# Performance work log

Hardware: AMD Instinct MI355X
Metric: run time of the kernel (lower is better)

The kernel has to match this reference:

```python
import jax, jax.numpy as jnp
import numpy as np

B, N = 4, 512
H, NH, L = 64, 4, 3
HD = H // NH          # 16
NODE_F, EDGE_F = 18, 7
H4 = H // 4           # 16
FF = 4 * H            # 256


def _ln(x, g, b, eps=1e-5):
    m = jnp.mean(x, axis=-1, keepdims=True)
    v = jnp.mean((x - m) ** 2, axis=-1, keepdims=True)
    return (x - m) * jax.lax.rsqrt(v + eps) * g + b


def _leaky(x):
    return jnp.where(x >= 0, x, 0.2 * x)


def _spd(edge_mask):
    # Vectorized Floyd-Warshall, mirrors GraphTransformer._compute_spd_matrix
    n = edge_mask.shape[1]
    spd = jnp.where(edge_mask, 1.0, float(n)).astype(jnp.float32)
    i = jnp.arange(n)
    spd = spd.at[:, i, i].set(0.0)
    def body(k, s):
        col = jax.lax.dynamic_slice_in_dim(s, k, 1, axis=2)  # [B,N,1]
        row = jax.lax.dynamic_slice_in_dim(s, k, 1, axis=1)  # [B,1,N]
        return jnp.minimum(s, col + row)
    return jax.lax.fori_loop(0, n, body, spd)


def setup_inputs() -> dict:
    key = jax.random.key(0)
    ks = iter(jax.random.split(key, 64))
    def nrm(shape, s):
        return jax.random.normal(next(ks), shape, jnp.float32) * s
    inp = {}
    inp["node_features"] = jax.random.normal(next(ks), (B, N, NODE_F), jnp.float32)
    inp["edge_features"] = jax.random.normal(next(ks), (B, N, N, EDGE_F), jnp.float32)
    nm = jax.random.uniform(next(ks), (B, N)) < 0.9
    inp["node_mask"] = nm.at[:, 0].set(True)
    inp["edge_mask"] = jax.random.uniform(next(ks), (B, N, N)) < 0.05
    s_h = 1.0 / np.sqrt(H)
    inp["node_proj_w"] = nrm((NODE_F, H), 0.2)
    inp["node_proj_b"] = jnp.zeros((H,), jnp.float32)
    inp["edge_proj_w"] = nrm((EDGE_F, H), 0.2)
    inp["edge_proj_b"] = jnp.zeros((H,), jnp.float32)
    inp["wq"] = nrm((L, H, H), s_h)
    inp["wk"] = nrm((L, H, H), s_h)
    inp["wv"] = nrm((L, H, H), s_h)
    inp["eb1_w"] = nrm((L, H, H4), s_h)
    inp["eb1_b"] = jnp.zeros((L, H4), jnp.float32)
    inp["eb_ln_g"] = jnp.ones((L, H4), jnp.float32)
    inp["eb_ln_b"] = jnp.zeros((L, H4), jnp.float32)
    inp["eb2_w"] = nrm((L, H4, NH), 0.2)
    inp["eb2_b"] = jnp.zeros((L, NH), jnp.float32)
    inp["spd1_w"] = nrm((L, 1, H4), 0.5)
    inp["spd1_b"] = jnp.zeros((L, H4), jnp.float32)
    inp["spd2_w"] = nrm((L, H4, NH), 0.2)
    inp["spd2_b"] = jnp.zeros((L, NH), jnp.float32)
    inp["wo_w"] = nrm((L, H, H), s_h)
    inp["wo_b"] = jnp.zeros((L, H), jnp.float32)
    inp["ln1_g"] = jnp.ones((L, H), jnp.float32)
    inp["ln1_b"] = jnp.zeros((L, H), jnp.float32)
    inp["ln2_g"] = jnp.ones((L, H), jnp.float32)
    inp["ln2_b"] = jnp.zeros((L, H), jnp.float32)
    inp["ffn1_w"] = nrm((L, H, FF), s_h)
    inp["ffn1_b"] = jnp.zeros((L, FF), jnp.float32)
    inp["ffn2_w"] = nrm((L, FF, H), 1.0 / np.sqrt(FF))
    inp["ffn2_b"] = jnp.zeros((L, H), jnp.float32)
    inp["score1_w"] = nrm((2 * H, H), 1.0 / np.sqrt(2 * H))
    inp["score1_b"] = jnp.zeros((H,), jnp.float32)
    inp["score_ln_g"] = jnp.ones((H,), jnp.float32)
    inp["score_ln_b"] = jnp.zeros((H,), jnp.float32)
    inp["score2_w"] = nrm((H, 1), 0.1)
    inp["score2_b"] = jnp.zeros((1,), jnp.float32)
    return inp


def reference(node_features, edge_features, node_mask, edge_mask,
              node_proj_w, node_proj_b, edge_proj_w, edge_proj_b,
              wq, wk, wv,
              eb1_w, eb1_b, eb_ln_g, eb_ln_b, eb2_w, eb2_b,
              spd1_w, spd1_b, spd2_w, spd2_b,
              wo_w, wo_b, ln1_g, ln1_b, ln2_g, ln2_b,
              ffn1_w, ffn1_b, ffn2_w, ffn2_b,
              score1_w, score1_b, score_ln_g, score_ln_b, score2_w, score2_b):
    NEG = -1000000000.0
    h = node_features @ node_proj_w + node_proj_b            # [B,N,H]
    e = edge_features @ edge_proj_w + edge_proj_b            # [B,N,N,H]
    spd = _spd(edge_mask)
    spd_n = (jnp.clip(spd, 0.0, 10.0) / 10.0)[..., None]      # [B,N,N,1]
    scale = 1.0 / np.sqrt(HD)
    for l in range(L):
        Q = (h @ wq[l]).reshape(B, N, NH, HD)
        K = (h @ wk[l]).reshape(B, N, NH, HD)
        V = (h @ wv[l]).reshape(B, N, NH, HD)
        scores = jnp.einsum('bihd,bjhd->bhij', Q, K) * scale  # [B,NH,N,N]
        x = _leaky(_ln(e @ eb1_w[l] + eb1_b[l], eb_ln_g[l], eb_ln_b[l]))
        edge_bias = jnp.transpose(x @ eb2_w[l] + eb2_b[l], (0, 3, 1, 2))
        sb = _leaky(spd_n @ spd1_w[l] + spd1_b[l]) @ spd2_w[l] + spd2_b[l]
        spd_bias = jnp.transpose(sb, (0, 3, 1, 2))
        bias = jnp.where(edge_mask[:, None, :, :], edge_bias, spd_bias)
        scores = jnp.where(node_mask[:, None, None, :], scores + bias, NEG)
        attn = jax.nn.softmax(scores, axis=-1)
        out = jnp.einsum('bhij,bjhd->bihd', attn, V).reshape(B, N, H)
        out = out @ wo_w[l] + wo_b[l]
        h = _ln(h + out, ln1_g[l], ln1_b[l])
        ff = jax.nn.gelu(h @ ffn1_w[l] + ffn1_b[l], approximate=False) @ ffn2_w[l] + ffn2_b[l]
        h = _ln(h + ff, ln2_g[l], ln2_b[l])
    h_ego = jnp.broadcast_to(h[:, :1, :], (B, N - 1, H))
    hc = jnp.concatenate([h_ego, h[:, 1:, :]], axis=-1)       # [B,N-1,2H]
    x = _leaky(_ln(hc @ score1_w + score1_b, score_ln_g, score_ln_b))
    logits = (x @ score2_w + score2_b)[..., 0]                # [B,N-1]
    cand_mask = node_mask[:, 1:]
    no_cand = ~jnp.any(cand_mask, axis=-1)
    cand_mask = cand_mask.at[:, 0].set(cand_mask[:, 0] | no_cand)
    logits = jnp.where(cand_mask, logits, NEG)
    probs = jax.nn.softmax(logits, axis=-1)
    return probs, h
```

## Files before the change

### kernel.cpp

```cpp
#include <hip/hip_runtime.h>
#include <math.h>

#define BB 4
#define NN 512
#define HH 64
#define NHH 4
#define HDD 16
#define LL 3
#define NNSQ 262144
#define FFF 256

__device__ __forceinline__ float wsum(float x) {
#pragma unroll
    for (int o = 1; o < 64; o <<= 1) x += __shfl_xor(x, o);
    return x;
}
__device__ __forceinline__ float wmaxr(float x) {
#pragma unroll
    for (int o = 1; o < 64; o <<= 1) x = fmaxf(x, __shfl_xor(x, o));
    return x;
}

__global__ void k_adj(const int* __restrict__ em, unsigned long long* __restrict__ adj,
                      unsigned int* __restrict__ blockCnt) {
    __shared__ unsigned int wc[4];
    int wv = threadIdx.x >> 6, lane = threadIdx.x & 63;
    int wid = blockIdx.x * 4 + wv;
    int chunk = wid & 7;
    int row = wid >> 3;
    int j = chunk * 64 + lane;
    int v = em[(size_t)row * NN + j];
    unsigned long long bal = __ballot(v != 0);
    if (lane == 0) { adj[row * 8 + chunk] = bal; wc[wv] = (unsigned int)__popcll(bal); }
    __syncthreads();
    if (threadIdx.x == 0) blockCnt[blockIdx.x] = wc[0] + wc[1] + wc[2] + wc[3];
}

__global__ void k_bfs(const unsigned long long* __restrict__ adj, unsigned char* __restrict__ spd) {
    __shared__ unsigned long long vis[8], fro[8], nxt[8];
    __shared__ unsigned long long dist8[64];
    unsigned char* dist = (unsigned char*)dist8;
    int t = threadIdx.x;
    int row = blockIdx.x;
    int b = row >> 9; int src = row & 511;
    dist8[t] = 0x0A0A0A0A0A0A0A0AULL;
    if (t < 8) { vis[t] = 0ULL; fro[t] = 0ULL; }
    __syncthreads();
    if (t == 0) {
        dist[src] = 0;
        vis[src >> 6] = 1ULL << (src & 63);
        fro[src >> 6] = 1ULL << (src & 63);
    }
    __syncthreads();
    const unsigned long long* arow = adj + (size_t)b * NN * 8;
    for (int d = 1; d <= 9; d++) {
        if (t < 8) nxt[t] = 0ULL;
        __syncthreads();
        int c = t >> 3, w = t & 7;
        unsigned long long f = fro[c];
        unsigned long long acc = 0ULL;
        while (f) {
            int k = (c << 6) + __builtin_ctzll(f);
            f &= f - 1;
            acc |= arow[k * 8 + w];
        }
        if (acc) atomicOr(&nxt[w], acc);
        __syncthreads();
        if (t < 8) {
            unsigned long long nw = nxt[t] & ~vis[t];
            vis[t] |= nw;
            fro[t] = nw;
            while (nw) {
                int j = (t << 6) + __builtin_ctzll(nw);
                nw &= nw - 1;
                dist[j] = (unsigned char)d;
            }
        }
        __syncthreads();
    }
    ((unsigned long long*)(spd + (size_t)row * NN))[t] = dist8[t];
}

__global__ __launch_bounds__(1024) void k_scan(const unsigned int* __restrict__ blockCnt,
                                               unsigned int* __restrict__ blockOff,
                                               unsigned int* __restrict__ counter) {
    __shared__ unsigned int part[1024];
    int t = threadIdx.x;
    unsigned int v0 = blockCnt[t * 4], v1 = blockCnt[t * 4 + 1],
                 v2 = blockCnt[t * 4 + 2], v3 = blockCnt[t * 4 + 3];
    unsigned int s = v0 + v1 + v2 + v3;
    part[t] = s;
    __syncthreads();
    for (int o = 1; o < 1024; o <<= 1) {
        unsigned int add = (t >= o) ? part[t - o] : 0u;
        __syncthreads();
        part[t] += add;
        __syncthreads();
    }
    unsigned int excl = part[t] - s;
    blockOff[t * 4]     = excl;
    blockOff[t * 4 + 1] = excl + v0;
    blockOff[t * 4 + 2] = excl + v0 + v1;
    blockOff[t * 4 + 3] = excl + v0 + v1 + v2;
    if (t == 1023) { counter[0] = part[t]; blockOff[4096] = part[t]; }
}

__global__ void k_scatter(const int* __restrict__ em, const unsigned int* __restrict__ blockOff,
                          unsigned int* __restrict__ elist) {
    __shared__ unsigned int wc[4];
    int t = threadIdx.x; int lane = t & 63; int wv = t >> 6;
    int idx = blockIdx.x * 256 + t;
    bool m = em[idx] != 0;
    unsigned long long bal = __ballot(m);
    if (lane == 0) wc[wv] = (unsigned int)__popcll(bal);
    __syncthreads();
    unsigned int base = blockOff[blockIdx.x];
    for (int w = 0; w < wv; w++) base += wc[w];
    if (m) {
        int pre = __popcll(bal & ((1ULL << lane) - 1ULL));
        elist[base + pre] = (unsigned int)idx;
    }
}

__global__ __launch_bounds__(256) void k_edge_bias(
    const float* __restrict__ ef, const unsigned int* __restrict__ counter,
    const unsigned int* __restrict__ elist,
    const float* __restrict__ epw, const float* __restrict__ epb,
    const float* __restrict__ eb1w, const float* __restrict__ eb1b,
    const float* __restrict__ lng, const float* __restrict__ lnb,
    const float* __restrict__ eb2w, const float* __restrict__ eb2b,
    float* __restrict__ vals) {
    unsigned int count = *counter;
    unsigned int idx = blockIdx.x * 256 + threadIdx.x;
    if (idx >= count) return;
    int l = blockIdx.y;
    unsigned int pos = elist[idx];
    const float* e7 = ef + (size_t)pos * 7;
    float f0 = e7[0], f1 = e7[1], f2 = e7[2], f3 = e7[3], f4 = e7[4], f5 = e7[5], f6 = e7[6];
    float tt[16];
#pragma unroll
    for (int c = 0; c < 16; c++) tt[c] = eb1b[l * 16 + c];
    const float* W1 = eb1w + l * 1024;
    for (int k = 0; k < 64; k++) {
        float ek = epb[k] + f0 * epw[k] + f1 * epw[64 + k] + f2 * epw[128 + k] + f3 * epw[192 + k]
                 + f4 * epw[256 + k] + f5 * epw[320 + k] + f6 * epw[384 + k];
#pragma unroll
        for (int c = 0; c < 16; c++) tt[c] += ek * W1[k * 16 + c];
    }
    float m = 0.f;
#pragma unroll
    for (int c = 0; c < 16; c++) m += tt[c];
    m *= 0.0625f;
    float var = 0.f;
#pragma unroll
    for (int c = 0; c < 16; c++) { float d = tt[c] - m; var += d * d; }
    var *= 0.0625f;
    float inv = rsqrtf(var + 1e-5f);
#pragma unroll
    for (int c = 0; c < 16; c++) {
        float x = (tt[c] - m) * inv * lng[l * 16 + c] + lnb[l * 16 + c];
        tt[c] = x >= 0.f ? x : 0.2f * x;
    }
#pragma unroll
    for (int hh = 0; hh < 4; hh++) {
        float a = eb2b[l * 4 + hh];
#pragma unroll
        for (int c = 0; c < 16; c++) a += tt[c] * eb2w[(l * 16 + c) * 4 + hh];
        vals[(unsigned int)((l * 4 + hh) << 16) + idx] = a;
    }
}

__global__ void k_node_proj(const float* __restrict__ nf, const float* __restrict__ w,
                            const float* __restrict__ bb, float* __restrict__ h) {
    int wid = blockIdx.x * 4 + (threadIdx.x >> 6);
    int f = threadIdx.x & 63;
    const float* r = nf + (size_t)wid * 18;
    float acc = bb[f];
#pragma unroll
    for (int c = 0; c < 18; c++) acc += r[c] * w[c * 64 + f];
    h[(size_t)wid * 64 + f] = acc;
}

__global__ __launch_bounds__(256) void k_qkvT(
    const float* __restrict__ h,
    const float* __restrict__ WQ, const float* __restrict__ WK, const float* __restrict__ WV,
    float* __restrict__ Q, float* __restrict__ KT, float* __restrict__ VT) {
    __shared__ float h_lds[16][64];
    int t = threadIdx.x;
    size_t base = (size_t)blockIdx.x * 16 * 64;
    for (int u = t; u < 1024; u += 256) ((float*)h_lds)[u] = h[base + u];
    __syncthreads();
    int wv = t >> 6, lane = t & 63;
    float aq[4] = {0,0,0,0}, ak[4] = {0,0,0,0}, av[4] = {0,0,0,0};
    for (int k = 0; k < 64; k++) {
        float wqv = WQ[k * 64 + lane], wkv = WK[k * 64 + lane], wvv = WV[k * 64 + lane];
#pragma unroll
        for (int r = 0; r < 4; r++) {
            float hv = h_lds[wv * 4 + r][k];
            aq[r] += hv * wqv; ak[r] += hv * wkv; av[r] += hv * wvv;
        }
    }
#pragma unroll
    for (int r = 0; r < 4; r++) {
        Q[base + (size_t)(wv * 4 + r) * 64 + lane] = aq[r];
    }
    int b = blockIdx.x >> 5;
    int j0 = (blockIdx.x & 31) * 16 + wv * 4;
    float4 kk; kk.x = ak[0]; kk.y = ak[1]; kk.z = ak[2]; kk.w = ak[3];
    float4 vv; vv.x = av[0]; vv.y = av[1]; vv.z = av[2]; vv.w = av[3];
    *(float4*)(KT + ((size_t)(b * 64 + lane)) * 512 + j0) = kk;
    *(float4*)(VT + ((size_t)(b * 64 + lane)) * 512 + j0) = vv;
}

__global__ __launch_bounds__(256) void k_attn3(
    const float* __restrict__ Q, const float* __restrict__ KT, const float* __restrict__ VT,
    const unsigned char* __restrict__ spd, const unsigned int* __restrict__ elist,
    const unsigned int* __restrict__ rowOff, const float* __restrict__ vals,
    const float* __restrict__ s1w, const float* __restrict__ s1b,
    const float* __restrict__ s2w, const float* __restrict__ s2b,
    const int* __restrict__ nmask, int l, float* __restrict__ attO) {
    __shared__ float kt[8192];
    __shared__ float bv[8192];
    __shared__ float tab[11];
    int bh = blockIdx.x;
    int b  = bh >> 2, hh = bh & 3;
    int i0 = blockIdx.y * 16;
    int t = threadIdx.x, wv = t >> 6, lane = t & 63;
    int rbase = i0 + wv * 4;
    float qv = Q[((size_t)(b * 512 + rbase + (lane >> 4))) * 64 + hh * 16 + (lane & 15)];
    float q[4][16];
#pragma unroll
    for (int r = 0; r < 4; r++)
#pragma unroll
        for (int d = 0; d < 16; d++)
            q[r][d] = __shfl(qv, r * 16 + d);
    const float4* ktg = (const float4*)(KT + (size_t)bh * 8192);
    float4* kts = (float4*)kt;
#pragma unroll
    for (int u = 0; u < 8; u++) kts[t + u * 256] = ktg[t + u * 256];
    if (t < 11) {
        float x = (float)t * 0.1f;
        float acc = s2b[l * 4 + hh];
#pragma unroll
        for (int c = 0; c < 16; c++) {
            float v = x * s1w[l * 16 + c] + s1b[l * 16 + c];
            v = v >= 0.f ? v : 0.2f * v;
            acc += v * s2w[(l * 16 + c) * 4 + hh];
        }
        tab[t] = acc;
    }
    __syncthreads();
    const unsigned char* sp = spd + ((size_t)(b * 512 + i0)) * 512;
#pragma unroll
    for (int u = 0; u < 8; u++) {
        int e4 = u * 1024 + t * 4;
        unsigned int w4 = *(const unsigned int*)(sp + e4);
        bv[e4 + 0] = tab[w4 & 255u];
        bv[e4 + 1] = tab[(w4 >> 8) & 255u];
        bv[e4 + 2] = tab[(w4 >> 16) & 255u];
        bv[e4 + 3] = tab[w4 >> 24];
    }
    __syncthreads();
    unsigned int vplane = (unsigned int)((l * 4 + hh) << 16);
#pragma unroll
    for (int rr = 0; rr < 4; rr++) {
        int g = b * 512 + rbase + rr;
        unsigned int e0 = rowOff[2 * g], e1 = rowOff[2 * g + 2];
        for (unsigned int e = e0 + lane; e < e1; e += 64) {
            int j = (int)(elist[e] & 511u);
            bv[(wv * 4 + rr) * 512 + j] = vals[vplane + e];
        }
    }
    __syncthreads();
    const int* nmb = nmask + b * 512;
    float sc[8][4];
    float mx[4] = {-3e38f, -3e38f, -3e38f, -3e38f};
#pragma unroll
    for (int c = 0; c < 8; c++) {
        int j = c * 64 + lane;
        float ktv[16];
#pragma unroll
        for (int d = 0; d < 16; d++) ktv[d] = kt[d * 512 + j];
        float madd = (nmb[j] != 0) ? 0.f : -1e9f;
#pragma unroll
        for (int r = 0; r < 4; r++) {
            float s = 0.f;
#pragma unroll
            for (int d = 0; d < 16; d++) s += q[r][d] * ktv[d];
            s = s * 0.25f + bv[(wv * 4 + r) * 512 + j] + madd;
            sc[c][r] = s;
            mx[r] = fmaxf(mx[r], s);
        }
    }
#pragma unroll
    for (int r = 0; r < 4; r++) mx[r] = wmaxr(mx[r]);
    float sm[4] = {0.f, 0.f, 0.f, 0.f};
#pragma unroll
    for (int c = 0; c < 8; c++)
#pragma unroll
        for (int r = 0; r < 4; r++) { sc[c][r] = __expf(sc[c][r] - mx[r]); sm[r] += sc[c][r]; }
#pragma unroll
    for (int r = 0; r < 4; r++) sm[r] = 1.0f / wsum(sm[r]);
#pragma unroll
    for (int c = 0; c < 8; c++)
#pragma unroll
        for (int r = 0; r < 4; r++) sc[c][r] *= sm[r];
    __syncthreads();
    const float4* vtg = (const float4*)(VT + (size_t)bh * 8192);
    float4* vts = (float4*)bv;
#pragma unroll
    for (int u = 0; u < 8; u++) vts[t + u * 256] = vtg[t + u * 256];
    __syncthreads();
    float acc[4][16];
#pragma unroll
    for (int r = 0; r < 4; r++)
#pragma unroll
        for (int d = 0; d < 16; d++) acc[r][d] = 0.f;
#pragma unroll
    for (int c = 0; c < 8; c++) {
        int j = c * 64 + lane;
#pragma unroll
        for (int d = 0; d < 16; d++) {
            float v = bv[d * 512 + j];
#pragma unroll
            for (int r = 0; r < 4; r++) acc[r][d] += sc[c][r] * v;
        }
    }
#pragma unroll
    for (int r = 0; r < 4; r++)
#pragma unroll
        for (int d = 0; d < 16; d++) {
            acc[r][d] += __shfl_xor(acc[r][d], 16);
            acc[r][d] += __shfl_xor(acc[r][d], 32);
        }
    __syncthreads();
    float* scr = kt + wv * 1040;
    if (lane < 16) {
#pragma unroll
        for (int r = 0; r < 4; r++)
#pragma unroll
            for (int d = 0; d < 16; d++) scr[lane * 65 + r * 16 + d] = acc[r][d];
    }
    float o = 0.f;
#pragma unroll
    for (int m = 0; m < 16; m++) o += scr[m * 65 + lane];
    attO[((size_t)(b * 512 + rbase + (lane >> 4))) * 64 + hh * 16 + (lane & 15)] = o;
}

__global__ __launch_bounds__(256) void k_oproj_ln1(
    const float* __restrict__ attO, const float* __restrict__ W, const float* __restrict__ Wb,
    const float* __restrict__ G, const float* __restrict__ Bt,
    float* __restrict__ h) {
    __shared__ float a_lds[4][64];
    int wv = threadIdx.x >> 6, lane = threadIdx.x & 63;
    int row = blockIdx.x * 4 + wv;
    a_lds[wv][lane] = attO[(size_t)row * 64 + lane];
    __syncthreads();
    float acc = Wb[lane];
#pragma unroll 8
    for (int k = 0; k < 64; k++) acc += a_lds[wv][k] * W[k * 64 + lane];
    float x = acc + h[(size_t)row * 64 + lane];
    float mn = wsum(x) * 0.015625f;
    float d = x - mn;
    float var = wsum(d * d) * 0.015625f;
    h[(size_t)row * 64 + lane] = d * rsqrtf(var + 1e-5f) * G[lane] + Bt[lane];
}

__global__ __launch_bounds__(256) void k_ffn(
    const float* __restrict__ W1, const float* __restrict__ B1,
    const float* __restrict__ W2, const float* __restrict__ B2,
    const float* __restrict__ G, const float* __restrict__ Bt,
    float* __restrict__ h) {
    __shared__ float h_lds[16][64];
    __shared__ float ff_lds[16][256];
    int t = threadIdx.x;
    size_t base = (size_t)blockIdx.x * 16 * 64;
    for (int u = t; u < 1024; u += 256) ((float*)h_lds)[u] = h[base + u];
    __syncthreads();
    int wv = t >> 6, lane = t & 63;
    float acc[4][4];
#pragma unroll
    for (int m = 0; m < 4; m++) {
        float bvv = B1[m * 64 + lane];
#pragma unroll
        for (int r = 0; r < 4; r++) acc[m][r] = bvv;
    }
    for (int k = 0; k < 64; k++) {
        float w0 = W1[k * 256 + lane], w1 = W1[k * 256 + 64 + lane],
              w2 = W1[k * 256 + 128 + lane], w3 = W1[k * 256 + 192 + lane];
#pragma unroll
        for (int r = 0; r < 4; r++) {
            float hv = h_lds[wv * 4 + r][k];
            acc[0][r] += hv * w0; acc[1][r] += hv * w1;
            acc[2][r] += hv * w2; acc[3][r] += hv * w3;
        }
    }
#pragma unroll
    for (int m = 0; m < 4; m++)
#pragma unroll
        for (int r = 0; r < 4; r++) {
            float u = acc[m][r];
            ff_lds[wv * 4 + r][m * 64 + lane] = 0.5f * u * (1.0f + erff(u * 0.70710678118654752f));
        }
    __syncthreads();
    float a2[4] = {0,0,0,0};
    for (int k = 0; k < 256; k++) {
        float w = W2[k * 64 + lane];
#pragma unroll
        for (int r = 0; r < 4; r++) a2[r] += ff_lds[wv * 4 + r][k] * w;
    }
    float b2v = B2[lane], gv = G[lane], btv = Bt[lane];
#pragma unroll
    for (int r = 0; r < 4; r++) {
        float x = a2[r] + b2v + h_lds[wv * 4 + r][lane];
        float mn = wsum(x) * 0.015625f;
        float d = x - mn;
        float var = wsum(d * d) * 0.015625f;
        h[base + (size_t)(wv * 4 + r) * 64 + lane] = d * rsqrtf(var + 1e-5f) * gv + btv;
    }
}

__global__ __launch_bounds__(256) void k_score(
    const float* __restrict__ h, const float* __restrict__ s1w, const float* __restrict__ s1b,
    const float* __restrict__ lng, const float* __restrict__ lnb,
    const float* __restrict__ s2w, const float* __restrict__ s2b,
    float* __restrict__ logits) {
    __shared__ float c_lds[4][128];
    int wv = threadIdx.x >> 6, lane = threadIdx.x & 63;
    int wid = blockIdx.x * 4 + wv;
    int b = wid / 511; int jj = wid % 511; int j = jj + 1;
    c_lds[wv][lane]      = h[((size_t)b * 512) * 64 + lane];
    c_lds[wv][64 + lane] = h[((size_t)(b * 512 + j)) * 64 + lane];
    __syncthreads();
    float acc = s1b[lane];
#pragma unroll 8
    for (int k = 0; k < 128; k++) acc += c_lds[wv][k] * s1w[k * 64 + lane];
    float mn = wsum(acc) * 0.015625f;
    float d = acc - mn;
    float var = wsum(d * d) * 0.015625f;
    float x = d * rsqrtf(var + 1e-5f) * lng[lane] + lnb[lane];
    x = x >= 0.f ? x : 0.2f * x;
    float p = wsum(x * s2w[lane]);
    if (lane == 0) logits[wid] = p + s2b[0];
}

__global__ __launch_bounds__(512) void k_probs(
    const float* __restrict__ logits, const int* __restrict__ nmask, float* __restrict__ out) {
    __shared__ float red[512];
    __shared__ int anyf;
    int b = blockIdx.x; int t = threadIdx.x;
    bool cand = false;
    if (t < 511) cand = nmask[b * 512 + 1 + t] != 0;
    if (t == 0) anyf = 0;
    __syncthreads();
    if (cand) atomicOr(&anyf, 1);
    __syncthreads();
    if (t == 0 && anyf == 0) cand = true;
    float val = -3e38f;
    if (t < 511) val = cand ? logits[b * 511 + t] : -1e9f;
    red[t] = val; __syncthreads();
    for (int s = 256; s > 0; s >>= 1) { if (t < s) red[t] = fmaxf(red[t], red[t + s]); __syncthreads(); }
    float m = red[0]; __syncthreads();
    float p = (t < 511) ? __expf(val - m) : 0.f;
    red[t] = p; __syncthreads();
    for (int s = 256; s > 0; s >>= 1) { if (t < s) red[t] += red[t + s]; __syncthreads(); }
    float inv = 1.0f / red[0];
    if (t < 511) out[b * 511 + t] = p * inv;
}

__global__ void k_copy_h(const float4* __restrict__ src, float4* __restrict__ dst) {
    int i = blockIdx.x * 256 + threadIdx.x;
    dst[i] = src[i];
}

extern "C" void kernel_launch(void* const* d_in, const int* in_sizes, int n_in,
                              void* d_out, int out_size, void* d_ws, size_t ws_size,
                              hipStream_t stream) {
    const float* nf    = (const float*)d_in[0];
    const float* ef    = (const float*)d_in[1];
    const int*   nm    = (const int*)d_in[2];
    const int*   em    = (const int*)d_in[3];
    const float* npw   = (const float*)d_in[4];
    const float* npb   = (const float*)d_in[5];
    const float* epw   = (const float*)d_in[6];
    const float* epb   = (const float*)d_in[7];
    const float* wq    = (const float*)d_in[8];
    const float* wk    = (const float*)d_in[9];
    const float* wv    = (const float*)d_in[10];
    const float* eb1w  = (const float*)d_in[11];
    const float* eb1b  = (const float*)d_in[12];
    const float* eblng = (const float*)d_in[13];
    const float* eblnb = (const float*)d_in[14];
    const float* eb2w  = (const float*)d_in[15];
    const float* eb2b  = (const float*)d_in[16];
    const float* s1wv  = (const float*)d_in[17];
    const float* s1bv  = (const float*)d_in[18];
    const float* s2wv  = (const float*)d_in[19];
    const float* s2bv  = (const float*)d_in[20];
    const float* wow   = (const float*)d_in[21];
    const float* wob   = (const float*)d_in[22];
    const float* ln1g  = (const float*)d_in[23];
    const float* ln1b  = (const float*)d_in[24];
    const float* ln2g  = (const float*)d_in[25];
    const float* ln2b  = (const float*)d_in[26];
    const float* f1w   = (const float*)d_in[27];
    const float* f1b   = (const float*)d_in[28];
    const float* f2w   = (const float*)d_in[29];
    const float* f2b   = (const float*)d_in[30];
    const float* sc1w  = (const float*)d_in[31];
    const float* sc1b  = (const float*)d_in[32];
    const float* sclng = (const float*)d_in[33];
    const float* sclnb = (const float*)d_in[34];
    const float* sc2w  = (const float*)d_in[35];
    const float* sc2b  = (const float*)d_in[36];

    char* W = (char*)d_ws;
    unsigned long long* adj     = (unsigned long long*)(W + 0);
    unsigned char*      spd     = (unsigned char*)(W + 131072);
    unsigned int*       counter = (unsigned int*)(W + 1179648);
    unsigned int*       elist   = (unsigned int*)(W + 1179904);
    float*              vals    = (float*)(W + 5374208);
    float*              hbuf    = (float*)(W + 8519936);
    float*              Qb      = (float*)(W + 9044224);
    float*              KTb     = (float*)(W + 9568512);
    float*              VTb     = (float*)(W + 10092800);
    float*              attO    = (float*)(W + 10617088);
    float*              logits  = (float*)(W + 11141376);
    unsigned int*       blockCnt= (unsigned int*)(W + 11149568);
    unsigned int*       blockOff= (unsigned int*)(W + 11165952);

    float* out = (float*)d_out;

    k_adj<<<4096, 256, 0, stream>>>(em, adj, blockCnt);
    k_bfs<<<2048, 64, 0, stream>>>(adj, spd);
    k_scan<<<1, 1024, 0, stream>>>(blockCnt, blockOff, counter);
    k_scatter<<<4096, 256, 0, stream>>>(em, blockOff, elist);
    k_edge_bias<<<dim3(256, 3), 256, 0, stream>>>(ef, counter, elist, epw, epb,
                                                  eb1w, eb1b, eblng, eblnb, eb2w, eb2b, vals);
    k_node_proj<<<512, 256, 0, stream>>>(nf, npw, npb, hbuf);

    for (int l = 0; l < LL; l++) {
        k_qkvT<<<128, 256, 0, stream>>>(hbuf, wq + l * 4096, wk + l * 4096, wv + l * 4096,
                                        Qb, KTb, VTb);
        k_attn3<<<dim3(16, 32), 256, 0, stream>>>(Qb, KTb, VTb, spd, elist, blockOff, vals,
                                                  s1wv, s1bv, s2wv, s2bv, nm, l, attO);
        k_oproj_ln1<<<512, 256, 0, stream>>>(attO, wow + l * 4096, wob + l * 64,
                                             ln1g + l * 64, ln1b + l * 64, hbuf);
        k_ffn<<<128, 256, 0, stream>>>(f1w + l * 16384, f1b + l * 256,
                                       f2w + l * 16384, f2b + l * 64,
                                       ln2g + l * 64, ln2b + l * 64, hbuf);
    }

    k_score<<<511, 256, 0, stream>>>(hbuf, sc1w, sc1b, sclng, sclnb, sc2w, sc2b, logits);
    k_copy_h<<<128, 256, 0, stream>>>((const float4*)hbuf, (float4*)(out + 2044));
    k_probs<<<4, 512, 0, stream>>>(logits, nm, out);
}
```

Measured before the change: 348.4 us.

## Fuse node projection, O-proj+LN1+FFN, output copy; widen BFS to 256 threads

The node projection is folded into the first-layer QKV kernel. The output projection with LayerNorm1 is merged into the FFN kernel, and the final copy of h is written directly from the last layer's FFN epilogue. Together these remove several kernel launches and global round-trips of the hidden state. The BFS kernel moves from 64 to 256 threads per block, scanning frontier bits per node instead of ctz loops over the frontier, and writes distances in parallel. The BFS change adds work proportional to all 512 nodes per level and more syncs, and the fused post kernel runs only 128 blocks.

New measurement: 366.6 us. 1.05x slower.

```diff
diff --git a/kernel.cpp b/kernel.cpp
--- a/kernel.cpp
+++ b/kernel.cpp
@@ -36,49 +36,46 @@
     if (threadIdx.x == 0) blockCnt[blockIdx.x] = wc[0] + wc[1] + wc[2] + wc[3];
 }
 
-__global__ void k_bfs(const unsigned long long* __restrict__ adj, unsigned char* __restrict__ spd) {
+__global__ __launch_bounds__(256) void k_bfs(const unsigned long long* __restrict__ adj,
+                                             unsigned char* __restrict__ spd) {
     __shared__ unsigned long long vis[8], fro[8], nxt[8];
     __shared__ unsigned long long dist8[64];
     unsigned char* dist = (unsigned char*)dist8;
     int t = threadIdx.x;
     int row = blockIdx.x;
     int b = row >> 9; int src = row & 511;
-    dist8[t] = 0x0A0A0A0A0A0A0A0AULL;
-    if (t < 8) { vis[t] = 0ULL; fro[t] = 0ULL; }
+    if (t < 64) dist8[t] = 0x0A0A0A0A0A0A0A0AULL;
+    if (t < 8) { vis[t] = 0ULL; fro[t] = 0ULL; nxt[t] = 0ULL; }
     __syncthreads();
     if (t == 0) {
         dist[src] = 0;
-        vis[src >> 6] = 1ULL << (src & 63);
-        fro[src >> 6] = 1ULL << (src & 63);
+        vis[src >> 6] |= 1ULL << (src & 63);
+        fro[src >> 6] |= 1ULL << (src & 63);
     }
     __syncthreads();
     const unsigned long long* arow = adj + (size_t)b * NN * 8;
+    int w = t & 7;
     for (int d = 1; d <= 9; d++) {
-        if (t < 8) nxt[t] = 0ULL;
-        __syncthreads();
-        int c = t >> 3, w = t & 7;
-        unsigned long long f = fro[c];
-        unsigned long long acc = 0ULL;
-        while (f) {
-            int k = (c << 6) + __builtin_ctzll(f);
-            f &= f - 1;
-            acc |= arow[k * 8 + w];
-        }
-        if (acc) atomicOr(&nxt[w], acc);
+        for (int k = t >> 3; k < 512; k += 32) {
+            if ((fro[k >> 6] >> (k & 63)) & 1ULL) {
+                unsigned long long m = arow[k * 8 + w];
+                if (m) atomicOr(&nxt[w], m);
+            }
+        }
         __syncthreads();
         if (t < 8) {
             unsigned long long nw = nxt[t] & ~vis[t];
             vis[t] |= nw;
             fro[t] = nw;
-            while (nw) {
-                int j = (t << 6) + __builtin_ctzll(nw);
-                nw &= nw - 1;
-                dist[j] = (unsigned char)d;
-            }
+            nxt[t] = 0ULL;
         }
         __syncthreads();
-    }
-    ((unsigned long long*)(spd + (size_t)row * NN))[t] = dist8[t];
+        for (int k = t; k < 512; k += 256) {
+            if ((fro[k >> 6] >> (k & 63)) & 1ULL) dist[k] = (unsigned char)d;
+        }
+        __syncthreads();
+    }
+    if (t < 64) ((unsigned long long*)(spd + (size_t)row * NN))[t] = dist8[t];
 }
 
 __global__ __launch_bounds__(1024) void k_scan(const unsigned int* __restrict__ blockCnt,
@@ -170,25 +167,30 @@
     }
 }
 
-__global__ void k_node_proj(const float* __restrict__ nf, const float* __restrict__ w,
-                            const float* __restrict__ bb, float* __restrict__ h) {
-    int wid = blockIdx.x * 4 + (threadIdx.x >> 6);
-    int f = threadIdx.x & 63;
-    const float* r = nf + (size_t)wid * 18;
-    float acc = bb[f];
-#pragma unroll
-    for (int c = 0; c < 18; c++) acc += r[c] * w[c * 64 + f];
-    h[(size_t)wid * 64 + f] = acc;
-}
-
 __global__ __launch_bounds__(256) void k_qkvT(
-    const float* __restrict__ h,
+    const float* __restrict__ h, const float* __restrict__ nf,
+    const float* __restrict__ npw, const float* __restrict__ npb,
     const float* __restrict__ WQ, const float* __restrict__ WK, const float* __restrict__ WV,
-    float* __restrict__ Q, float* __restrict__ KT, float* __restrict__ VT) {
+    float* __restrict__ Q, float* __restrict__ KT, float* __restrict__ VT,
+    float* __restrict__ hOut, int first) {
     __shared__ float h_lds[16][64];
+    __shared__ float nf_lds[16][18];
     int t = threadIdx.x;
     size_t base = (size_t)blockIdx.x * 16 * 64;
-    for (int u = t; u < 1024; u += 256) ((float*)h_lds)[u] = h[base + u];
+    if (first) {
+        for (int u = t; u < 288; u += 256) nf_lds[u / 18][u % 18] = nf[(size_t)blockIdx.x * 288 + u];
+        __syncthreads();
+        for (int u = t; u < 1024; u += 256) {
+            int row = u >> 6, col = u & 63;
+            float acc = npb[col];
+#pragma unroll
+            for (int c = 0; c < 18; c++) acc += nf_lds[row][c] * npw[c * 64 + col];
+            h_lds[row][col] = acc;
+            hOut[base + u] = acc;
+        }
+    } else {
+        for (int u = t; u < 1024; u += 256) ((float*)h_lds)[u] = h[base + u];
+    }
     __syncthreads();
     int wv = t >> 6, lane = t & 63;
     float aq[4] = {0,0,0,0}, ak[4] = {0,0,0,0}, av[4] = {0,0,0,0};
@@ -347,37 +349,38 @@
     attO[((size_t)(b * 512 + rbase + (lane >> 4))) * 64 + hh * 16 + (lane & 15)] = o;
 }
 
-__global__ __launch_bounds__(256) void k_oproj_ln1(
-    const float* __restrict__ attO, const float* __restrict__ W, const float* __restrict__ Wb,
-    const float* __restrict__ G, const float* __restrict__ Bt,
-    float* __restrict__ h) {
-    __shared__ float a_lds[4][64];
-    int wv = threadIdx.x >> 6, lane = threadIdx.x & 63;
-    int row = blockIdx.x * 4 + wv;
-    a_lds[wv][lane] = attO[(size_t)row * 64 + lane];
-    __syncthreads();
-    float acc = Wb[lane];
-#pragma unroll 8
-    for (int k = 0; k < 64; k++) acc += a_lds[wv][k] * W[k * 64 + lane];
-    float x = acc + h[(size_t)row * 64 + lane];
-    float mn = wsum(x) * 0.015625f;
-    float d = x - mn;
-    float var = wsum(d * d) * 0.015625f;
-    h[(size_t)row * 64 + lane] = d * rsqrtf(var + 1e-5f) * G[lane] + Bt[lane];
-}
-
-__global__ __launch_bounds__(256) void k_ffn(
+__global__ __launch_bounds__(256) void k_post(
+    const float* __restrict__ attO,
+    const float* __restrict__ Wo, const float* __restrict__ Wob,
+    const float* __restrict__ G1, const float* __restrict__ B1n,
     const float* __restrict__ W1, const float* __restrict__ B1,
     const float* __restrict__ W2, const float* __restrict__ B2,
-    const float* __restrict__ G, const float* __restrict__ Bt,
-    float* __restrict__ h) {
+    const float* __restrict__ G2, const float* __restrict__ Bt2,
+    float* __restrict__ h, float* __restrict__ outH) {
+    __shared__ float a_lds[16][64];
     __shared__ float h_lds[16][64];
     __shared__ float ff_lds[16][256];
     int t = threadIdx.x;
     size_t base = (size_t)blockIdx.x * 16 * 64;
-    for (int u = t; u < 1024; u += 256) ((float*)h_lds)[u] = h[base + u];
+    for (int u = t; u < 1024; u += 256) {
+        ((float*)a_lds)[u] = attO[base + u];
+        ((float*)h_lds)[u] = h[base + u];
+    }
     __syncthreads();
     int wv = t >> 6, lane = t & 63;
+#pragma unroll
+    for (int rr = 0; rr < 4; rr++) {
+        int row = wv * 4 + rr;
+        float acc = Wob[lane];
+#pragma unroll 8
+        for (int k = 0; k < 64; k++) acc += a_lds[row][k] * Wo[k * 64 + lane];
+        float x = acc + h_lds[row][lane];
+        float mn = wsum(x) * 0.015625f;
+        float d = x - mn;
+        float var = wsum(d * d) * 0.015625f;
+        h_lds[row][lane] = d * rsqrtf(var + 1e-5f) * G1[lane] + B1n[lane];
+    }
+    __syncthreads();
     float acc[4][4];
 #pragma unroll
     for (int m = 0; m < 4; m++) {
@@ -409,14 +412,17 @@
 #pragma unroll
         for (int r = 0; r < 4; r++) a2[r] += ff_lds[wv * 4 + r][k] * w;
     }
-    float b2v = B2[lane], gv = G[lane], btv = Bt[lane];
+    float b2v = B2[lane], gv = G2[lane], btv = Bt2[lane];
 #pragma unroll
     for (int r = 0; r < 4; r++) {
         float x = a2[r] + b2v + h_lds[wv * 4 + r][lane];
         float mn = wsum(x) * 0.015625f;
         float d = x - mn;
         float var = wsum(d * d) * 0.015625f;
-        h[base + (size_t)(wv * 4 + r) * 64 + lane] = d * rsqrtf(var + 1e-5f) * gv + btv;
+        float res = d * rsqrtf(var + 1e-5f) * gv + btv;
+        size_t o = base + (size_t)(wv * 4 + r) * 64 + lane;
+        h[o] = res;
+        if (outH) outH[o] = res;
     }
 }
 
@@ -466,11 +472,6 @@
     for (int s = 256; s > 0; s >>= 1) { if (t < s) red[t] += red[t + s]; __syncthreads(); }
     float inv = 1.0f / red[0];
     if (t < 511) out[b * 511 + t] = p * inv;
-}
-
-__global__ void k_copy_h(const float4* __restrict__ src, float4* __restrict__ dst) {
-    int i = blockIdx.x * 256 + threadIdx.x;
-    dst[i] = src[i];
 }
 
 extern "C" void kernel_launch(void* const* d_in, const int* in_sizes, int n_in,
@@ -532,26 +533,26 @@
     float* out = (float*)d_out;
 
     k_adj<<<4096, 256, 0, stream>>>(em, adj, blockCnt);
-    k_bfs<<<2048, 64, 0, stream>>>(adj, spd);
+    k_bfs<<<2048, 256, 0, stream>>>(adj, spd);
     k_scan<<<1, 1024, 0, stream>>>(blockCnt, blockOff, counter);
     k_scatter<<<4096, 256, 0, stream>>>(em, blockOff, elist);
     k_edge_bias<<<dim3(256, 3), 256, 0, stream>>>(ef, counter, elist, epw, epb,
                                                   eb1w, eb1b, eblng, eblnb, eb2w, eb2b, vals);
-    k_node_proj<<<512, 256, 0, stream>>>(nf, npw, npb, hbuf);
 
     for (int l = 0; l < LL; l++) {
-        k_qkvT<<<128, 256, 0, stream>>>(hbuf, wq + l * 4096, wk + l * 4096, wv + l * 4096,
-                                        Qb, KTb, VTb);
+        k_qkvT<<<128, 256, 0, stream>>>(hbuf, nf, npw, npb,
+                                        wq + l * 4096, wk + l * 4096, wv + l * 4096,
+                                        Qb, KTb, VTb, hbuf, l == 0 ? 1 : 0);
         k_attn3<<<dim3(16, 32), 256, 0, stream>>>(Qb, KTb, VTb, spd, elist, blockOff, vals,
                                                   s1wv, s1bv, s2wv, s2bv, nm, l, attO);
-        k_oproj_ln1<<<512, 256, 0, stream>>>(attO, wow + l * 4096, wob + l * 64,
-                                             ln1g + l * 64, ln1b + l * 64, hbuf);
-        k_ffn<<<128, 256, 0, stream>>>(f1w + l * 16384, f1b + l * 256,
-                                       f2w + l * 16384, f2b + l * 64,
-                                       ln2g + l * 64, ln2b + l * 64, hbuf);
+        k_post<<<128, 256, 0, stream>>>(attO, wow + l * 4096, wob + l * 64,
+                                        ln1g + l * 64, ln1b + l * 64,
+                                        f1w + l * 16384, f1b + l * 256,
+                                        f2w + l * 16384, f2b + l * 64,
+                                        ln2g + l * 64, ln2b + l * 64,
+                                        hbuf, l == LL - 1 ? (out + 2044) : (float*)nullptr);
     }
 
     k_score<<<511, 256, 0, stream>>>(hbuf, sc1w, sc1b, sclng, sclnb, sc2w, sc2b, logits);
-    k_copy_h<<<128, 256, 0, stream>>>((const float4*)hbuf, (float4*)(out + 2044));
     k_probs<<<4, 512, 0, stream>>>(logits, nm, out);
 }
```
